# Kernel tuning notes

Hardware: AMD Instinct MI355X
Metric: run time of the kernel (lower is better)

Reference implementation:

```python
import jax, jax.numpy as jnp
import numpy as np
import math

B, N, D, H = 32, 577, 768, 12
HD = D // H  # 64
WS = 24  # window size
NUM_REL_DIST = (2 * WS - 1) * (2 * WS - 1) + 3  # 2212


def _build_rel_pos_index():
    ch, cw = np.arange(WS), np.arange(WS)
    coords = np.stack(np.meshgrid(ch, cw, indexing='ij'))  # [2, WS, WS]
    cf = coords.reshape(2, -1)  # [2, WS*WS]
    rel = cf[:, :, None] - cf[:, None, :]  # [2, WS*WS, WS*WS]
    rel = rel.transpose(1, 2, 0).astype(np.int64)
    rel[:, :, 0] += WS - 1
    rel[:, :, 1] += WS - 1
    rel[:, :, 0] *= 2 * WS - 1
    idx = np.zeros((WS * WS + 1, WS * WS + 1), dtype=np.int64)
    idx[1:, 1:] = rel.sum(-1)
    idx[0, 0:] = NUM_REL_DIST - 3
    idx[0:, 0] = NUM_REL_DIST - 2
    idx[0, 0] = NUM_REL_DIST - 1
    return idx.astype(np.int32)


def setup_inputs() -> dict:
    key = jax.random.key(0)
    ks = jax.random.split(key, 7)
    s = 1.0 / math.sqrt(D)
    return {
        'hidden_states': jax.random.normal(ks[0], (B, N, D), jnp.float32),
        'q_w': jax.random.normal(ks[1], (D, D), jnp.float32) * s,
        'q_b': jax.random.normal(ks[2], (D,), jnp.float32) * 0.02,
        'k_w': jax.random.normal(ks[3], (D, D), jnp.float32) * s,
        'v_w': jax.random.normal(ks[4], (D, D), jnp.float32) * s,
        'v_b': jax.random.normal(ks[5], (D,), jnp.float32) * 0.02,
        'rel_pos_table': jax.random.normal(ks[6], (NUM_REL_DIST, H), jnp.float32) * 0.02,
        'rel_pos_index': jnp.asarray(_build_rel_pos_index()),
    }


def reference(hidden_states, q_w, q_b, k_w, v_w, v_b, rel_pos_table, rel_pos_index):
    # QKV projections (torch Linear: x @ W.T + b); key has no bias
    q = hidden_states @ q_w.T + q_b  # [B,N,D]
    k = hidden_states @ k_w.T        # [B,N,D]
    v = hidden_states @ v_w.T + v_b  # [B,N,D]

    def heads(x):
        return x.reshape(B, N, H, HD).transpose(0, 2, 1, 3)  # [B,H,N,HD]

    q, k, v = heads(q), heads(k), heads(v)
    scores = jnp.einsum('bhqd,bhkd->bhqk', q, k) / math.sqrt(HD)
    # relative position bias: table lookup -> [N,N,H] -> [H,N,N]
    bias = rel_pos_table[rel_pos_index.reshape(-1)].reshape(N, N, H)
    scores = scores + bias.transpose(2, 0, 1)[None]
    probs = jax.nn.softmax(scores, axis=-1)  # dropout p=0 (eval)
    ctx = jnp.einsum('bhqk,bhkd->bhqd', probs, v)
    return ctx.transpose(0, 2, 1, 3).reshape(B, N, D)
```

## Files before the change

kernel.cpp:

```cpp
#include <hip/hip_runtime.h>
#include <hip/hip_bf16.h>

#define B_  32
#define N_  577
#define D_  768
#define H_  12
#define HD_ 64
#define M_  (B_ * N_)
#define NW_ (3 * D_)
#define VN_ 640
#define BPAD_ 640
#define SCALE_ 0.18033688f

typedef __bf16 bf16_t;
typedef __bf16 bf16x8 __attribute__((ext_vector_type(8)));
typedef __bf16 bf16x4 __attribute__((ext_vector_type(4)));
typedef float  f32x4  __attribute__((ext_vector_type(4)));

static __device__ __forceinline__ bf16x8 ldg8(const bf16_t* p) {
    return *reinterpret_cast<const bf16x8*>(p);
}

#define GPERM(r) (((r) & 32) | (((r) & 8) << 1) | (((r) & 4) << 1) | \
                  (((r) & 16) >> 2) | ((r) & 3))

#define GLOAD_LDS16(g, l)                                                     \
    __builtin_amdgcn_global_load_lds(                                         \
        (const __attribute__((address_space(1))) void*)(g),                   \
        (__attribute__((address_space(3))) void*)(l), 16, 0, 0)

__global__ void cvt_f32_bf16(const float* __restrict__ src,
                             bf16_t* __restrict__ dst, int n4) {
    int i = blockIdx.x * blockDim.x + threadIdx.x;
    if (i < n4) {
        float4 f = reinterpret_cast<const float4*>(src)[i];
        bf16x4 o;
        o.x = (bf16_t)f.x; o.y = (bf16_t)f.y; o.z = (bf16_t)f.z; o.w = (bf16_t)f.w;
        *reinterpret_cast<bf16x4*>(dst + (size_t)i * 4) = o;
    }
}

__global__ void cvt3_f32_bf16(const float* __restrict__ s0,
                              const float* __restrict__ s1,
                              const float* __restrict__ s2,
                              bf16_t* __restrict__ dst, int n4) {
    int i = blockIdx.x * blockDim.x + threadIdx.x;
    if (i < n4) {
        const float* src = blockIdx.y == 0 ? s0 : (blockIdx.y == 1 ? s1 : s2);
        float4 f = reinterpret_cast<const float4*>(src)[i];
        bf16x4 o;
        o.x = (bf16_t)f.x; o.y = (bf16_t)f.y; o.z = (bf16_t)f.z; o.w = (bf16_t)f.w;
        *reinterpret_cast<bf16x4*>(dst + (size_t)blockIdx.y * n4 * 4 + (size_t)i * 4) = o;
    }
}

__global__ void build_bias2(const float* __restrict__ table,
                            const int* __restrict__ idx,
                            float* __restrict__ bias2) {
    int q = blockIdx.x;
    int rr = q < N_ ? q : (N_ - 1);
    for (int kl = threadIdx.x; kl < BPAD_; kl += blockDim.x) {
        int s = kl & 63;
        int gk = (kl & ~63) | GPERM(s);
        if (gk < N_) {
            int id = idx[rr * N_ + gk];
            const float* trow = table + (size_t)id * H_;
#pragma unroll
            for (int h = 0; h < H_; ++h)
                bias2[((size_t)h * BPAD_ + q) * BPAD_ + kl] =
                    trow[h] * 1.44269504f;
        } else {
#pragma unroll
            for (int h = 0; h < H_; ++h)
                bias2[((size_t)h * BPAD_ + q) * BPAD_ + kl] = -1e30f;
        }
    }
}

__global__ __launch_bounds__(512, 2) void qkv_gemm(
    const bf16_t* __restrict__ hb, const bf16_t* __restrict__ W,
    const float* __restrict__ qb, const float* __restrict__ vb,
    bf16_t* __restrict__ Q, bf16_t* __restrict__ K, bf16_t* __restrict__ VT)
{
    __shared__ __align__(16) char lds[131072];

    int tid = threadIdx.x;
    int w  = tid >> 6, l = tid & 63;
    int lr = l & 15, lg = l >> 4;
    int wm = w >> 2, wn = w & 3;

    int wg = blockIdx.x;
    int xcd = wg & 7, pos = wg >> 3;
    int base = (xcd == 0) ? 0 : 83 + (xcd - 1) * 82;
    int wgid = base + pos;
    int bx = wgid / 9, ct = wgid - bx * 9;
    int brow = bx * 256;
    int mat = ct / 3, csub = ct - mat * 3;
    int cbase = csub * 256;

    int srow = tid >> 2;
    int sslot = (tid & 3) ^ ((srow >> 1) & 3);
    const bf16_t* pa[2];
    const bf16_t* pb[2];
#pragma unroll
    for (int r = 0; r < 2; ++r) {
        int ra = brow + r * 128 + srow; ra = ra < M_ ? ra : (M_ - 1);
        pa[r] = hb + (size_t)ra * D_ + sslot * 8;
        pb[r] = W + (size_t)(ct * 256 + r * 128 + srow) * D_ + sslot * 8;
    }

    auto stage = [&](int buf, int k) {
#pragma unroll
        for (int r = 0; r < 2; ++r) {
            GLOAD_LDS16(pa[r] + k, lds + buf * 16384 + r * 8192 + tid * 16);
            GLOAD_LDS16(pb[r] + k, lds + 65536 + buf * 16384 + r * 8192 + tid * 16);
        }
    };

    f32x4 acc[8][4] = {};
    stage(0, 0);
    stage(1, 32);
    stage(2, 64);
    int xsw = (lr >> 1) & 3;

#pragma unroll 4
    for (int t = 0; t < 24; ++t) {
        if (t < 22)       asm volatile("s_waitcnt vmcnt(8)" ::: "memory");
        else if (t == 22) asm volatile("s_waitcnt vmcnt(4)" ::: "memory");
        else              asm volatile("s_waitcnt vmcnt(0)" ::: "memory");
        __builtin_amdgcn_s_barrier();
        __builtin_amdgcn_sched_barrier(0);
        if (t + 3 < 24) stage((t + 3) & 3, (t + 3) * 32);
        __builtin_amdgcn_sched_barrier(0);

        const char* pA = lds + (t & 3) * 16384;
        const char* pB = lds + 65536 + (t & 3) * 16384;
        bf16x8 bf[4];
#pragma unroll
        for (int n = 0; n < 4; ++n) {
            int row = wn * 64 + n * 16 + lr;
            bf[n] = *reinterpret_cast<const bf16x8*>(
                pB + row * 64 + ((lg ^ xsw) << 4));
        }
        __builtin_amdgcn_s_setprio(1);
#pragma unroll
        for (int m = 0; m < 8; ++m) {
            int row = wm * 128 + m * 16 + lr;
            bf16x8 af = *reinterpret_cast<const bf16x8*>(
                pA + row * 64 + ((lg ^ xsw) << 4));
#pragma unroll
            for (int n = 0; n < 4; ++n)
                acc[m][n] = __builtin_amdgcn_mfma_f32_16x16x32_bf16(
                    af, bf[n], acc[m][n], 0, 0, 0);
        }
        __builtin_amdgcn_s_setprio(0);
        __builtin_amdgcn_sched_barrier(0);
    }
    __syncthreads();

    bf16_t* ep = (bf16_t*)lds;
    if (mat < 2) {
        bf16_t* dst0 = (mat == 0) ? Q : K;
#pragma unroll
        for (int hp = 0; hp < 2; ++hp) {
            if (wm == hp) {
#pragma unroll
                for (int m = 0; m < 8; ++m)
#pragma unroll
                    for (int n = 0; n < 4; ++n) {
                        int col = wn * 64 + n * 16 + lr;
                        float badd = (mat == 0) ? qb[cbase + col] : 0.f;
#pragma unroll
                        for (int j = 0; j < 4; ++j) {
                            int rl = m * 16 + lg * 4 + j;
                            float v = acc[m][n][j];
                            v = (mat == 0) ? (v + badd) * SCALE_ : v;
                            ep[rl * 260 + col] = (bf16_t)v;
                        }
                    }
            }
            __syncthreads();
#pragma unroll
            for (int k = 0; k < 8; ++k) {
                int c = k * 512 + tid;
                int row = c >> 5, chunk = c & 31;
                int col0 = chunk * 8;
                int grow = brow + hp * 128 + row;
                if (grow < M_) {
                    int bb = grow / N_, nn = grow - bb * N_;
                    int hh = csub * 4 + (col0 >> 6);
                    int hd0 = col0 & 63;
                    *reinterpret_cast<bf16x8*>(
                        dst0 + ((size_t)(bb * H_ + hh) * N_ + nn) * HD_ + hd0) =
                        *reinterpret_cast<const bf16x8*>(ep + row * 260 + col0);
                }
            }
            __syncthreads();
        }
    } else {
#pragma unroll
        for (int hp = 0; hp < 2; ++hp) {
            if (wm == hp) {
#pragma unroll
                for (int m = 0; m < 8; ++m)
#pragma unroll
                    for (int n = 0; n < 4; ++n) {
                        int col = wn * 64 + n * 16 + lr;
                        float badd = vb[cbase + col];
#pragma unroll
                        for (int j = 0; j < 4; ++j) {
                            int rl = m * 16 + lg * 4 + j;
                            ep[col * 132 + rl] = (bf16_t)(acc[m][n][j] + badd);
                        }
                    }
            }
            __syncthreads();
#pragma unroll
            for (int k = 0; k < 8; ++k) {
                int c = k * 512 + tid;
                int col = c >> 4, rc = c & 15;
                int grow0 = brow + hp * 128 + rc * 8;
                int hh = csub * 4 + (col >> 6), hd = col & 63;
                int bb = grow0 / N_, nn0 = grow0 - bb * N_;
                if (nn0 + 8 <= N_ && grow0 + 8 <= M_) {
                    *reinterpret_cast<bf16x8*>(
                        VT + ((size_t)(bb * H_ + hh) * HD_ + hd) * VN_ + nn0) =
                        *reinterpret_cast<const bf16x8*>(ep + col * 132 + rc * 8);
                } else {
                    for (int jj = 0; jj < 8; ++jj) {
                        int grow = grow0 + jj;
                        if (grow >= M_) break;
                        int b2 = grow / N_, n2 = grow - b2 * N_;
                        VT[((size_t)(b2 * H_ + hh) * HD_ + hd) * VN_ + n2] =
                            ep[col * 132 + rc * 8 + jj];
                    }
                }
            }
            __syncthreads();
        }
    }
}

__global__ __launch_bounds__(256) void attn(
    const bf16_t* __restrict__ Q, const bf16_t* __restrict__ K,
    const bf16_t* __restrict__ VT, const float* __restrict__ bias2,
    float* __restrict__ out)
{
    __shared__ __align__(16) char Kl[2][8192];
    __shared__ __align__(16) char Vl[2][8192];

    int tid = threadIdx.x;
    int w = tid >> 6, l = tid & 63, lr = l & 15, lg = l >> 4;

    int wg = blockIdx.x;
    int wgid = (wg & 7) * 480 + (wg >> 3);
    int h = wgid / 320;
    int rem = wgid - h * 320;
    int b = rem / 10;
    int qt = rem - b * 10;

    const bf16_t* Qp = Q  + (size_t)(b * H_ + h) * N_ * HD_;
    const bf16_t* Kp = K  + (size_t)(b * H_ + h) * N_ * HD_;
    const bf16_t* Vp = VT + (size_t)(b * H_ + h) * HD_ * VN_;
    const float*  bp = bias2 + (size_t)h * BPAD_ * BPAD_;

    int q0 = qt * 64 + w * 16;
    int qrow = q0 + lr;
    int qrow_c = qrow < N_ ? qrow : (N_ - 1);
    bf16x8 aQ0 = ldg8(Qp + (size_t)qrow_c * HD_ + lg * 8);
    bf16x8 aQ1 = ldg8(Qp + (size_t)qrow_c * HD_ + 32 + lg * 8);

    bf16x8 vone;
#pragma unroll
    for (int i = 0; i < 8; ++i) vone[i] = (bf16_t)1.0f;

    int rloc = l >> 3;
    int cswz = (l & 7) ^ rloc;
    const bf16_t* Kst[2];
    const bf16_t* Vst[2];
#pragma unroll
    for (int rnd = 0; rnd < 2; ++rnd) {
        int r = rnd * 32 + w * 8 + rloc;
        int gk = GPERM(r);
        Kst[rnd] = Kp + (size_t)gk * HD_ + cswz * 8;
        Vst[rnd] = Vp + (size_t)r * VN_ + cswz * 8;
    }

    f32x4 o[4] = {};
    f32x4 osum = {};
    const int NT = 10;

    auto stageKV = [&](int buf, int k0) {
#pragma unroll
        for (int rnd = 0; rnd < 2; ++rnd)
            GLOAD_LDS16(Kst[rnd] + (size_t)k0 * HD_,
                        Kl[buf] + rnd * 4096 + w * 1024);
#pragma unroll
        for (int rnd = 0; rnd < 2; ++rnd)
            GLOAD_LDS16(Vst[rnd] + k0, Vl[buf] + rnd * 4096 + w * 1024);
    };
    auto loadBias = [&](int k0, f32x4* bbv) {
        const float* brow = bp + (size_t)(q0 + lr) * BPAD_ + k0;
#pragma unroll
        for (int kt = 0; kt < 4; ++kt)
            bbv[kt] = *reinterpret_cast<const f32x4*>(brow + kt * 16 + lg * 4);
    };

    auto tile = [&](int t, int rbuf, const f32x4* bbcur, f32x4* bbnxt) {
        int k0 = t * 64;
        if (t + 1 < NT) {
            stageKV(rbuf ^ 1, k0 + 64);
            loadBias(k0 + 64, bbnxt);
        }
        __builtin_amdgcn_sched_barrier(0);

        f32x4 s[4];
        __builtin_amdgcn_s_setprio(1);
#pragma unroll
        for (int kt = 0; kt < 4; ++kt) {
            int r = kt * 16 + lr;
            bf16x8 kf0 = *reinterpret_cast<const bf16x8*>(
                Kl[rbuf] + r * 128 + ((lg ^ (r & 7)) << 4));
            bf16x8 kf1 = *reinterpret_cast<const bf16x8*>(
                Kl[rbuf] + r * 128 + (((4 + lg) ^ (r & 7)) << 4));
            f32x4 a = __builtin_amdgcn_mfma_f32_16x16x32_bf16(
                kf0, aQ0, bbcur[kt], 0, 0, 0);
            s[kt] = __builtin_amdgcn_mfma_f32_16x16x32_bf16(kf1, aQ1, a, 0, 0, 0);
        }
        __builtin_amdgcn_s_setprio(0);

        float p[4][4];
#pragma unroll
        for (int kt = 0; kt < 4; ++kt)
#pragma unroll
            for (int j = 0; j < 4; ++j)
                p[kt][j] = __builtin_amdgcn_exp2f(s[kt][j]);

        __builtin_amdgcn_s_setprio(1);
#pragma unroll
        for (int kc = 0; kc < 2; ++kc) {
            bf16x8 aP;
            aP[0] = (bf16_t)p[2 * kc][0];
            aP[1] = (bf16_t)p[2 * kc][1];
            aP[2] = (bf16_t)p[2 * kc][2];
            aP[3] = (bf16_t)p[2 * kc][3];
            aP[4] = (bf16_t)p[2 * kc + 1][0];
            aP[5] = (bf16_t)p[2 * kc + 1][1];
            aP[6] = (bf16_t)p[2 * kc + 1][2];
            aP[7] = (bf16_t)p[2 * kc + 1][3];
            osum = __builtin_amdgcn_mfma_f32_16x16x32_bf16(aP, vone, osum, 0, 0, 0);
#pragma unroll
            for (int ft = 0; ft < 4; ++ft) {
                int d = ft * 16 + lr;
                bf16x8 bV = *reinterpret_cast<const bf16x8*>(
                    Vl[rbuf] + d * 128 + (((kc * 4 + lg) ^ (d & 7)) << 4));
                o[ft] = __builtin_amdgcn_mfma_f32_16x16x32_bf16(aP, bV, o[ft], 0, 0, 0);
            }
        }
        __builtin_amdgcn_s_setprio(0);
        __builtin_amdgcn_sched_barrier(0);

        if (t + 1 < NT) asm volatile("s_waitcnt vmcnt(4)" ::: "memory");
        else            asm volatile("s_waitcnt vmcnt(0)" ::: "memory");
        __builtin_amdgcn_s_barrier();
        __builtin_amdgcn_sched_barrier(0);
    };

    f32x4 bbA[4], bbB[4];
    stageKV(0, 0);
    loadBias(0, bbA);
    asm volatile("s_waitcnt vmcnt(4)" ::: "memory");
    __builtin_amdgcn_s_barrier();
    __builtin_amdgcn_sched_barrier(0);

    for (int tp = 0; tp < NT / 2; ++tp) {
        tile(tp * 2,     0, bbA, bbB);
        tile(tp * 2 + 1, 1, bbB, bbA);
    }

#pragma unroll
    for (int j = 0; j < 4; ++j) {
        int row = q0 + lg * 4 + j;
        if (row < N_) {
            float inv = 1.f / osum[j];
#pragma unroll
            for (int ft = 0; ft < 4; ++ft)
                out[((size_t)(b * N_ + row)) * D_ + h * HD_ + ft * 16 + lr] =
                    o[ft][j] * inv;
        }
    }
}

extern "C" void kernel_launch(void* const* d_in, const int* in_sizes, int n_in,
                              void* d_out, int out_size, void* d_ws, size_t ws_size,
                              hipStream_t stream)
{
    const float* hs    = (const float*)d_in[0];
    const float* q_w   = (const float*)d_in[1];
    const float* q_b   = (const float*)d_in[2];
    const float* k_w   = (const float*)d_in[3];
    const float* v_w   = (const float*)d_in[4];
    const float* v_b   = (const float*)d_in[5];
    const float* table = (const float*)d_in[6];
    const int*   rpi   = (const int*)d_in[7];
    float* out = (float*)d_out;

    char* ws = (char*)d_ws;
    size_t off = 0;
    auto alloc = [&](size_t bytes) {
        char* p = ws + off;
        off = (off + bytes + 255) & ~(size_t)255;
        return p;
    };
    bf16_t* hb  = (bf16_t*)alloc((size_t)M_ * D_ * 2);
    bf16_t* Wc  = (bf16_t*)alloc((size_t)NW_ * D_ * 2);
    bf16_t* Qb  = (bf16_t*)alloc((size_t)B_ * H_ * N_ * HD_ * 2);
    bf16_t* Kb  = (bf16_t*)alloc((size_t)B_ * H_ * N_ * HD_ * 2 + 16384);
    bf16_t* VTb = (bf16_t*)alloc((size_t)B_ * H_ * HD_ * VN_ * 2);
    float*  bia = (float*)alloc((size_t)H_ * BPAD_ * BPAD_ * 4);

    int n4h = M_ * D_ / 4;
    cvt_f32_bf16<<<(n4h + 255) / 256, 256, 0, stream>>>(hs, hb, n4h);
    int n4w = D_ * D_ / 4;
    cvt3_f32_bf16<<<dim3((n4w + 255) / 256, 3), 256, 0, stream>>>(
        q_w, k_w, v_w, Wc, n4w);
    build_bias2<<<BPAD_, 256, 0, stream>>>(table, rpi, bia);

    qkv_gemm<<<657, 512, 0, stream>>>(hb, Wc, q_b, v_b, Qb, Kb, VTb);

    attn<<<3840, 256, 0, stream>>>(Qb, Kb, VTb, bia, out);
}
```

Measured before the change: 211.2 us.

## Halve QKV GEMM M-tile to 128 rows and use triple-buffered LDS

Shrinks the QKV projection GEMM tile from 256x256 to 128x256, doubling the workgroup count, and drops from four to three LDS stages, cutting shared memory from 128KB to 72KB. The aim is better CU fill on the small grid (657 blocks previously) and less tail imbalance, plus a simpler single-pass epilogue. The cost is lower arithmetic intensity per tile (more reloads of the weight tile), a shallower prefetch pipeline, and a launch-bounds hint of 4 blocks per CU that likely cannot be met with 72KB of LDS each.

```diff
diff --git a/kernel.cpp b/kernel.cpp
--- a/kernel.cpp
+++ b/kernel.cpp
@@ -77,12 +77,12 @@
     }
 }
 
-__global__ __launch_bounds__(512, 2) void qkv_gemm(
+__global__ __launch_bounds__(512, 4) void qkv_gemm(
     const bf16_t* __restrict__ hb, const bf16_t* __restrict__ W,
     const float* __restrict__ qb, const float* __restrict__ vb,
     bf16_t* __restrict__ Q, bf16_t* __restrict__ K, bf16_t* __restrict__ VT)
 {
-    __shared__ __align__(16) char lds[131072];
+    __shared__ __align__(16) char lds[73728];
 
     int tid = threadIdx.x;
     int w  = tid >> 6, l = tid & 63;
@@ -91,50 +91,45 @@
 
     int wg = blockIdx.x;
     int xcd = wg & 7, pos = wg >> 3;
-    int base = (xcd == 0) ? 0 : 83 + (xcd - 1) * 82;
+    int base = (xcd == 0) ? 0 : 164 + (xcd - 1) * 163;
     int wgid = base + pos;
     int bx = wgid / 9, ct = wgid - bx * 9;
-    int brow = bx * 256;
+    int brow = bx * 128;
     int mat = ct / 3, csub = ct - mat * 3;
     int cbase = csub * 256;
 
     int srow = tid >> 2;
     int sslot = (tid & 3) ^ ((srow >> 1) & 3);
-    const bf16_t* pa[2];
+    int ra = brow + srow; ra = ra < M_ ? ra : (M_ - 1);
+    const bf16_t* pa = hb + (size_t)ra * D_ + sslot * 8;
     const bf16_t* pb[2];
 #pragma unroll
-    for (int r = 0; r < 2; ++r) {
-        int ra = brow + r * 128 + srow; ra = ra < M_ ? ra : (M_ - 1);
-        pa[r] = hb + (size_t)ra * D_ + sslot * 8;
+    for (int r = 0; r < 2; ++r)
         pb[r] = W + (size_t)(ct * 256 + r * 128 + srow) * D_ + sslot * 8;
-    }
 
     auto stage = [&](int buf, int k) {
-#pragma unroll
-        for (int r = 0; r < 2; ++r) {
-            GLOAD_LDS16(pa[r] + k, lds + buf * 16384 + r * 8192 + tid * 16);
-            GLOAD_LDS16(pb[r] + k, lds + 65536 + buf * 16384 + r * 8192 + tid * 16);
-        }
+        GLOAD_LDS16(pa + k, lds + buf * 8192 + tid * 16);
+#pragma unroll
+        for (int r = 0; r < 2; ++r)
+            GLOAD_LDS16(pb[r] + k, lds + 24576 + buf * 16384 + r * 8192 + tid * 16);
     };
 
-    f32x4 acc[8][4] = {};
+    f32x4 acc[4][4] = {};
     stage(0, 0);
     stage(1, 32);
-    stage(2, 64);
     int xsw = (lr >> 1) & 3;
 
-#pragma unroll 4
+#pragma unroll 3
     for (int t = 0; t < 24; ++t) {
-        if (t < 22)       asm volatile("s_waitcnt vmcnt(8)" ::: "memory");
-        else if (t == 22) asm volatile("s_waitcnt vmcnt(4)" ::: "memory");
-        else              asm volatile("s_waitcnt vmcnt(0)" ::: "memory");
+        if (t < 23) asm volatile("s_waitcnt vmcnt(3)" ::: "memory");
+        else        asm volatile("s_waitcnt vmcnt(0)" ::: "memory");
         __builtin_amdgcn_s_barrier();
         __builtin_amdgcn_sched_barrier(0);
-        if (t + 3 < 24) stage((t + 3) & 3, (t + 3) * 32);
-        __builtin_amdgcn_sched_barrier(0);
-
-        const char* pA = lds + (t & 3) * 16384;
-        const char* pB = lds + 65536 + (t & 3) * 16384;
+        if (t + 2 < 24) stage((t + 2) % 3, (t + 2) * 32);
+        __builtin_amdgcn_sched_barrier(0);
+
+        const char* pA = lds + (t % 3) * 8192;
+        const char* pB = lds + 24576 + (t % 3) * 16384;
         bf16x8 bf[4];
 #pragma unroll
         for (int n = 0; n < 4; ++n) {
@@ -144,8 +139,8 @@
         }
         __builtin_amdgcn_s_setprio(1);
 #pragma unroll
-        for (int m = 0; m < 8; ++m) {
-            int row = wm * 128 + m * 16 + lr;
+        for (int m = 0; m < 4; ++m) {
+            int row = wm * 64 + m * 16 + lr;
             bf16x8 af = *reinterpret_cast<const bf16x8*>(
                 pA + row * 64 + ((lg ^ xsw) << 4));
 #pragma unroll
@@ -162,81 +157,69 @@
     if (mat < 2) {
         bf16_t* dst0 = (mat == 0) ? Q : K;
 #pragma unroll
-        for (int hp = 0; hp < 2; ++hp) {
-            if (wm == hp) {
-#pragma unroll
-                for (int m = 0; m < 8; ++m)
-#pragma unroll
-                    for (int n = 0; n < 4; ++n) {
-                        int col = wn * 64 + n * 16 + lr;
-                        float badd = (mat == 0) ? qb[cbase + col] : 0.f;
-#pragma unroll
-                        for (int j = 0; j < 4; ++j) {
-                            int rl = m * 16 + lg * 4 + j;
-                            float v = acc[m][n][j];
-                            v = (mat == 0) ? (v + badd) * SCALE_ : v;
-                            ep[rl * 260 + col] = (bf16_t)v;
-                        }
-                    }
-            }
-            __syncthreads();
-#pragma unroll
-            for (int k = 0; k < 8; ++k) {
-                int c = k * 512 + tid;
-                int row = c >> 5, chunk = c & 31;
-                int col0 = chunk * 8;
-                int grow = brow + hp * 128 + row;
-                if (grow < M_) {
-                    int bb = grow / N_, nn = grow - bb * N_;
-                    int hh = csub * 4 + (col0 >> 6);
-                    int hd0 = col0 & 63;
-                    *reinterpret_cast<bf16x8*>(
-                        dst0 + ((size_t)(bb * H_ + hh) * N_ + nn) * HD_ + hd0) =
-                        *reinterpret_cast<const bf16x8*>(ep + row * 260 + col0);
+        for (int m = 0; m < 4; ++m)
+#pragma unroll
+            for (int n = 0; n < 4; ++n) {
+                int col = wn * 64 + n * 16 + lr;
+                float badd = (mat == 0) ? qb[cbase + col] : 0.f;
+#pragma unroll
+                for (int j = 0; j < 4; ++j) {
+                    int rl = wm * 64 + m * 16 + lg * 4 + j;
+                    float v = acc[m][n][j];
+                    v = (mat == 0) ? (v + badd) * SCALE_ : v;
+                    ep[rl * 260 + col] = (bf16_t)v;
                 }
             }
-            __syncthreads();
+        __syncthreads();
+#pragma unroll
+        for (int k = 0; k < 8; ++k) {
+            int c = k * 512 + tid;
+            int row = c >> 5, chunk = c & 31;
+            int col0 = chunk * 8;
+            int grow = brow + row;
+            if (grow < M_) {
+                int bb = grow / N_, nn = grow - bb * N_;
+                int hh = csub * 4 + (col0 >> 6);
+                int hd0 = col0 & 63;
+                *reinterpret_cast<bf16x8*>(
+                    dst0 + ((size_t)(bb * H_ + hh) * N_ + nn) * HD_ + hd0) =
+                    *reinterpret_cast<const bf16x8*>(ep + row * 260 + col0);
+            }
         }
     } else {
 #pragma unroll
-        for (int hp = 0; hp < 2; ++hp) {
-            if (wm == hp) {
-#pragma unroll
-                for (int m = 0; m < 8; ++m)
-#pragma unroll
-                    for (int n = 0; n < 4; ++n) {
-                        int col = wn * 64 + n * 16 + lr;
-                        float badd = vb[cbase + col];
-#pragma unroll
-                        for (int j = 0; j < 4; ++j) {
-                            int rl = m * 16 + lg * 4 + j;
-                            ep[col * 132 + rl] = (bf16_t)(acc[m][n][j] + badd);
-                        }
-                    }
-            }
-            __syncthreads();
-#pragma unroll
-            for (int k = 0; k < 8; ++k) {
-                int c = k * 512 + tid;
-                int col = c >> 4, rc = c & 15;
-                int grow0 = brow + hp * 128 + rc * 8;
-                int hh = csub * 4 + (col >> 6), hd = col & 63;
-                int bb = grow0 / N_, nn0 = grow0 - bb * N_;
-                if (nn0 + 8 <= N_ && grow0 + 8 <= M_) {
-                    *reinterpret_cast<bf16x8*>(
-                        VT + ((size_t)(bb * H_ + hh) * HD_ + hd) * VN_ + nn0) =
-                        *reinterpret_cast<const bf16x8*>(ep + col * 132 + rc * 8);
-                } else {
-                    for (int jj = 0; jj < 8; ++jj) {
-                        int grow = grow0 + jj;
-                        if (grow >= M_) break;
-                        int b2 = grow / N_, n2 = grow - b2 * N_;
-                        VT[((size_t)(b2 * H_ + hh) * HD_ + hd) * VN_ + n2] =
-                            ep[col * 132 + rc * 8 + jj];
-                    }
+        for (int m = 0; m < 4; ++m)
+#pragma unroll
+            for (int n = 0; n < 4; ++n) {
+                int col = wn * 64 + n * 16 + lr;
+                float badd = vb[cbase + col];
+#pragma unroll
+                for (int j = 0; j < 4; ++j) {
+                    int rl = wm * 64 + m * 16 + lg * 4 + j;
+                    ep[col * 132 + rl] = (bf16_t)(acc[m][n][j] + badd);
                 }
             }
-            __syncthreads();
+        __syncthreads();
+#pragma unroll
+        for (int k = 0; k < 8; ++k) {
+            int c = k * 512 + tid;
+            int col = c >> 4, rc = c & 15;
+            int grow0 = brow + rc * 8;
+            int hh = csub * 4 + (col >> 6), hd = col & 63;
+            int bb = grow0 / N_, nn0 = grow0 - bb * N_;
+            if (nn0 + 8 <= N_ && grow0 + 8 <= M_) {
+                *reinterpret_cast<bf16x8*>(
+                    VT + ((size_t)(bb * H_ + hh) * HD_ + hd) * VN_ + nn0) =
+                    *reinterpret_cast<const bf16x8*>(ep + col * 132 + rc * 8);
+            } else {
+                for (int jj = 0; jj < 8; ++jj) {
+                    int grow = grow0 + jj;
+                    if (grow >= M_) break;
+                    int b2 = grow / N_, n2 = grow - b2 * N_;
+                    VT[((size_t)(b2 * H_ + hh) * HD_ + hd) * VN_ + n2] =
+                        ep[col * 132 + rc * 8 + jj];
+                }
+            }
         }
     }
 }
@@ -426,7 +409,7 @@
         q_w, k_w, v_w, Wc, n4w);
     build_bias2<<<BPAD_, 256, 0, stream>>>(table, rpi, bia);
 
-    qkv_gemm<<<657, 512, 0, stream>>>(hb, Wc, q_b, v_b, Qb, Kb, VTb);
+    qkv_gemm<<<1305, 512, 0, stream>>>(hb, Wc, q_b, v_b, Qb, Kb, VTb);
 
     attn<<<3840, 256, 0, stream>>>(Qb, Kb, VTb, bia, out);
 }
```

Result: slower. 226.6 us (+7.3%).
